# Kernel tuning notes

Measured on AMD Instinct MI355X. Metric: run time of the kernel, lower is better.

## Reference

```python
import jax, jax.numpy as jnp
import numpy as np

SEQ, B, OBS, H = 128, 256, 64, 1024

def setup_inputs() -> dict:
    key = jax.random.key(0)
    ks = jax.random.split(key, 16)
    s = 0.03  # keep weights small so tanh/sigmoid stay in a sane range
    n = lambda k, shape, sc=s: jax.random.normal(k, shape, jnp.float32) * sc
    return {
        "x": jax.random.normal(ks[0], (SEQ * B, OBS), jnp.float32),
        "done": jax.random.randint(ks[1], (SEQ * B,), 0, 2).astype(jnp.int32),
        "h0": n(ks[2], (2, B, H), 0.1),
        "c0": n(ks[3], (2, B, H), 0.1),
        "W_ih0": n(ks[4], (4 * H, OBS)),
        "W_hh0": n(ks[5], (4 * H, H)),
        "b_ih0": jnp.zeros((4 * H,), jnp.float32),
        "b_hh0": jnp.zeros((4 * H,), jnp.float32),
        "W_ih1": n(ks[6], (4 * H, H)),
        "W_hh1": n(ks[7], (4 * H, H)),
        "b_ih1": jnp.zeros((4 * H,), jnp.float32),
        "b_hh1": jnp.zeros((4 * H,), jnp.float32),
        "ln_g": jnp.ones((H,), jnp.float32),
        "ln_b": jnp.zeros((H,), jnp.float32),
        "W1": n(ks[8], (512, H)),
        "b1": jnp.zeros((512,), jnp.float32),
        "W2": n(ks[9], (128, 512)),
        "b2": jnp.zeros((128,), jnp.float32),
        "W3": n(ks[10], (64, 128)),
        "b3": jnp.zeros((64,), jnp.float32),
        "Wv": n(ks[11], (1, 64)),
        "bv": jnp.zeros((1,), jnp.float32),
    }

def _lstm_cell(xin, h, c, Wih, Whh, bih, bhh):
    # PyTorch gate order: input, forget, cell(g), output
    g = xin @ Wih.T + bih + h @ Whh.T + bhh
    i, f, gg, o = jnp.split(g, 4, axis=-1)
    c2 = jax.nn.sigmoid(f) * c + jax.nn.sigmoid(i) * jnp.tanh(gg)
    h2 = jax.nn.sigmoid(o) * jnp.tanh(c2)
    return h2, c2

def reference(x, done, h0, c0, W_ih0, W_hh0, b_ih0, b_hh0, W_ih1, W_hh1,
              b_ih1, b_hh1, ln_g, ln_b, W1, b1, W2, b2, W3, b3, Wv, bv):
    batch = h0.shape[1]
    obs = x.shape[-1]
    xs = x.reshape(-1, batch, obs)                      # (S, B, obs)
    ds = done.reshape(-1, batch).astype(x.dtype)        # (S, B)

    def step(carry, td):
        h, c = carry                                    # each (2, B, H)
        xt, dt = td
        m = (1.0 - dt)[:, None]                         # reset mask (B, 1)
        h0_, c0_ = _lstm_cell(xt, h[0] * m, c[0] * m, W_ih0, W_hh0, b_ih0, b_hh0)
        h1_, c1_ = _lstm_cell(h0_, h[1] * m, c[1] * m, W_ih1, W_hh1, b_ih1, b_hh1)
        return (jnp.stack([h0_, h1_]), jnp.stack([c0_, c1_])), h1_

    (hN, cN), hs = jax.lax.scan(step, (h0, c0), (xs, ds))
    hidden = hs.reshape(-1, hs.shape[-1])               # (S*B, H)

    # LayerNorm (eps = 1e-5, torch default)
    mu = hidden.mean(-1, keepdims=True)
    var = jnp.mean(jnp.square(hidden - mu), -1, keepdims=True)
    hn = (hidden - mu) * jax.lax.rsqrt(var + 1e-5) * ln_g + ln_b

    a = jax.nn.elu(hn @ W1.T + b1)
    a = jax.nn.elu(a @ W2.T + b2)
    a = jax.nn.elu(a @ W3.T + b3)
    value = a @ Wv.T + bv                               # (S*B, 1)
    return value, hN, cN
```

## Files before the change

kernel.cpp:

```cpp
#include <hip/hip_runtime.h>
#include <cstdint>
#include <cstddef>

typedef unsigned short u16;
typedef __attribute__((ext_vector_type(8))) short short8;
typedef __attribute__((ext_vector_type(4))) float f32x4;

#define SEQ 128
#define BATCH 256
#define HID 1024
#define LSZ 262144

#define MFMA(a,b,c) __builtin_amdgcn_mfma_f32_16x16x32_bf16((a),(b),(c),0,0,0)

#define GLDS_CG(g, l) __builtin_amdgcn_global_load_lds( \
  (__attribute__((address_space(1))) void*)(uintptr_t)(const void*)(g), \
  (__attribute__((address_space(3))) void*)(unsigned)(uintptr_t)(void*)(l), 16, 0, 17)
#define GLDS_NC(g, l) __builtin_amdgcn_global_load_lds( \
  (__attribute__((address_space(1))) void*)(uintptr_t)(const void*)(g), \
  (__attribute__((address_space(3))) void*)(unsigned)(uintptr_t)(void*)(l), 16, 0, 0)

__device__ __forceinline__ u16 f2b(float f) {
  union { float f; unsigned u; } v; v.f = f;
  unsigned r = (v.u + 0x7FFFu + ((v.u >> 16) & 1u)) >> 16;
  return (u16)r;
}
__device__ __forceinline__ float b2f(u16 h) {
  union { unsigned u; float f; } v; v.u = ((unsigned)h) << 16; return v.f;
}
__device__ __forceinline__ float sigm(float x){ return 1.f/(1.f + __expf(-x)); }
__device__ __forceinline__ float tanh_f(float x){
  x = fminf(15.f, fmaxf(-15.f, x));
  float e = __expf(2.f*x); return (e-1.f)/(e+1.f);
}
__device__ __forceinline__ float eluf(float x){ return x > 0.f ? x : expm1f(x); }

__device__ __forceinline__ void store_cg(u16* p, short8 v) {
  asm volatile("global_store_dwordx4 %0, %1, off sc0 sc1" :: "v"(p), "v"(v) : "memory");
}
__device__ __forceinline__ void wait_vm0() {
  asm volatile("s_waitcnt vmcnt(0)" ::: "memory");
}
__device__ __forceinline__ void waitgroup(int* f, int tgt) {
  if (threadIdx.x < 64) {
    int idx = threadIdx.x & 31;
    while (__hip_atomic_load(f + idx, __ATOMIC_RELAXED, __HIP_MEMORY_SCOPE_AGENT) < tgt)
      __builtin_amdgcn_s_sleep(1);
  }
  __syncthreads();
}

static const size_t OFF_W0F  = 0;
static const size_t OFF_W1F  = 8912896;
static const size_t OFF_XF   = 25690112;
static const size_t OFF_H0U  = 29884416;
static const size_t OFF_C0   = 30932992;
static const size_t OFF_C1   = 31981568;
static const size_t OFF_H1U  = 33030144;
static const size_t OFF_BS0  = 100663296;
static const size_t OFF_BS1  = 100679680;
static const size_t OFF_MU   = 100697088;
static const size_t OFF_RSTD = 100828160;
static const size_t OFF_W1LN = 100959232;
static const size_t OFF_S1   = 102007808;
static const size_t OFF_B1P  = 102009856;
static const size_t OFF_W2B  = 102011904;
static const size_t OFF_W3B  = 102142976;
static const size_t OFF_A1   = 102159360;
static const size_t OFF_A2   = 0;
static const size_t OFF_A3   = 8912896;
static const size_t OFF_H0M  = 102159360;
static const size_t OFF_H1M  = 102159360 + 1048576;

__global__ void prep_wf(const float* __restrict__ wih, const float* __restrict__ whh,
                        u16* __restrict__ out, int nkb, int kx) {
  int b = blockIdx.x; int cg = b >> 3, ct = b & 7;
  int g = ct >> 1;
  int n = nkb << 9;
  for (int e = threadIdx.x; e < n; e += 256) {
    int kb = e >> 9, r = e & 511;
    int q = r >> 7, col16 = (r >> 3) & 15, j = r & 7;
    int hl = (ct & 1) * 16 + col16;
    int gr = g * HID + cg * 32 + hl;
    int k = kb * 32 + q * 8 + j;
    float w = (k < kx) ? wih[(size_t)gr * kx + k] : whh[(size_t)gr * HID + (k - kx)];
    out[((size_t)(cg * nkb + kb) * 8 + ct) * 512 + r] = f2b(w);
  }
}

__global__ void prep_w1ln(const float* __restrict__ w1, const float* __restrict__ lng,
                          const float* __restrict__ lnb, const float* __restrict__ b1,
                          u16* __restrict__ w1ln, float* __restrict__ S1, float* __restrict__ b1p) {
  int j = blockIdx.x;
  float s = 0.f, bb = 0.f;
  for (int k = threadIdx.x; k < HID; k += 256) {
    float w = w1[(size_t)j * HID + k];
    u16 q = f2b(w * lng[k]);
    w1ln[(size_t)j * HID + k] = q;
    s += b2f(q);
    bb += w * lnb[k];
  }
  __shared__ float r1[256], r2[256];
  r1[threadIdx.x] = s; r2[threadIdx.x] = bb;
  __syncthreads();
  for (int o = 128; o > 0; o >>= 1) {
    if (threadIdx.x < (unsigned)o) { r1[threadIdx.x] += r1[threadIdx.x+o]; r2[threadIdx.x] += r2[threadIdx.x+o]; }
    __syncthreads();
  }
  if (threadIdx.x == 0) { S1[j] = r1[0]; b1p[j] = b1[j] + r2[0]; }
}

__global__ void prep_misc(const float* bih0, const float* bhh0, const float* bih1, const float* bhh1,
                          const float* x, const float* h0in, const float* c0in,
                          const float* w2, const float* w3, const int* done,
                          float* bs0, float* bs1, u16* xf, u16* h0m, u16* h1m,
                          float* c0buf, float* c1buf, u16* w2b, u16* w3b, int* flg) {
  size_t i = (size_t)blockIdx.x * blockDim.x + threadIdx.x;
  if (i < 4096) { bs0[i] = bih0[i] + bhh0[i]; return; }
  i -= 4096;
  if (i < 4096) { bs1[i] = bih1[i] + bhh1[i]; return; }
  i -= 4096;
  if (i < 2097152) {
    int o = (int)i;
    int r = o & 511, tile = o >> 9;
    int q = r >> 7, rl = (r >> 3) & 15, j = r & 7;
    int kb = tile & 1, v = tile >> 1;
    int grt = v & 15, t = v >> 4;
    int row = grt * 16 + rl, k = kb * 32 + q * 8 + j;
    xf[o] = f2b(x[((size_t)t * BATCH + row) * 64 + k]);
    return;
  }
  i -= 2097152;
  if (i < 262144) {
    int o = (int)i;
    int r = o & 511, tile = o >> 9;
    int q = r >> 7, rl = (r >> 3) & 15, j = r & 7;
    int grt = tile >> 5, kb = tile & 31;
    int row = grt * 16 + rl, h = kb * 32 + q * 8 + j;
    h0m[o] = done[row] ? (u16)0 : f2b(h0in[(size_t)row * HID + h]);
    return;
  }
  i -= 262144;
  if (i < 262144) {
    int o = (int)i;
    int r = o & 511, tile = o >> 9;
    int q = r >> 7, rl = (r >> 3) & 15, j = r & 7;
    int grt = tile >> 5, kb = tile & 31;
    int row = grt * 16 + rl, h = kb * 32 + q * 8 + j;
    h1m[o] = done[row] ? (u16)0 : f2b(h0in[LSZ + (size_t)row * HID + h]);
    return;
  }
  i -= 262144;
  if (i < LSZ) { c0buf[i] = c0in[i]; return; }
  i -= LSZ;
  if (i < LSZ) { c1buf[i] = c0in[LSZ + i]; return; }
  i -= LSZ;
  if (i < 65536) { w2b[i] = f2b(w2[i]); return; }
  i -= 65536;
  if (i < 8192) { w3b[i] = f2b(w3[i]); return; }
  i -= 8192;
  if (i < 512) { flg[i] = 0; return; }
}

__global__ __launch_bounds__(256, 2) void lstm_persist(
    const u16* __restrict__ w0f, const u16* __restrict__ w1f, const u16* __restrict__ xf,
    u16* __restrict__ h0u, u16* __restrict__ h1u,
    u16* __restrict__ h0m, u16* __restrict__ h1m,
    float* __restrict__ c0b, float* __restrict__ c1b,
    const float* __restrict__ bs0, const float* __restrict__ bs1,
    const int* __restrict__ done, int* __restrict__ flg,
    float* __restrict__ dout)
{
  const int bid = blockIdx.x;
  const int layer = bid >> 8;
  const int rg = (bid >> 5) & 7;
  const int cg = bid & 31;
  const int tid = threadIdx.x;
  const int lane = tid & 63, wv = tid >> 6;
  const int quad = lane >> 4, c16 = lane & 15;
  const int NKB = layer ? 64 : 34;
  const int NC  = layer ? 16 : 9;
  const u16* Wf = layer ? w1f : w0f;
  const float* bs = layer ? bs1 : bs0;
  float* cb = layer ? c1b : c0b;
  int* fl0 = flg;
  int* fl1 = flg + 256;
  int* myf = (layer ? fl1 : fl0) + rg * 32 + cg;
  int* g0 = fl0 + rg * 32;
  int* g1 = fl1 + rg * 32;

  __shared__ __align__(16) u16 smem[16384];
  float* gl = (float*)smem;

  const short8 z8 = {0,0,0,0,0,0,0,0};

  for (int t = 0; t < SEQ; ++t) {
    if (layer == 0) {
      if (t >= 1) waitgroup(g0, t);
    } else {
      if (t >= 1) waitgroup(g1, t);
    }

    auto ocmap = [&](int p) -> int {
      if (layer) return p >= 16 ? 7 : (p < 8 ? p + 8 : p - 8);
      return p > 8 ? 8 : p;
    };

    auto issueA = [&](int p) {
      int oc = ocmap(p);
      int kb = oc * 4 + wv; if (kb > NKB - 1) kb = NKB - 1;
      u16* lb = &smem[((unsigned)(p & 3)) * 4096 + (unsigned)wv * 1024];
      if (layer == 0) {
        if (kb < 2) {
          #pragma unroll
          for (int j = 0; j < 2; ++j) {
            const u16* g = xf + ((size_t)((t * 16 + rg * 2 + j) * 2 + kb)) * 512 + lane * 8;
            GLDS_NC(g, lb + j * 512);
          }
        } else {
          #pragma unroll
          for (int j = 0; j < 2; ++j) {
            const u16* g = h0m + (size_t)(t & 1) * 262144
                               + (size_t)((rg * 2 + j) * 32 + (kb - 2)) * 512 + lane * 8;
            GLDS_CG(g, lb + j * 512);
          }
        }
      } else {
        if (kb < 32) {
          #pragma unroll
          for (int j = 0; j < 2; ++j) {
            const u16* g = h0u + (size_t)((t + 1) & 1) * 262144
                               + (size_t)((rg * 2 + j) * 32 + kb) * 512 + lane * 8;
            GLDS_CG(g, lb + j * 512);
          }
        } else {
          #pragma unroll
          for (int j = 0; j < 2; ++j) {
            const u16* g = h1m + (size_t)(t & 1) * 262144
                               + (size_t)((rg * 2 + j) * 32 + (kb - 32)) * 512 + lane * 8;
            GLDS_CG(g, lb + j * 512);
          }
        }
      }
    };

    auto loadB = [&](int p, short8 (&vB)[4][2]) {
      int oc = ocmap(p);
      #pragma unroll
      for (int kbl = 0; kbl < 4; ++kbl) {
        int kb = oc * 4 + kbl; if (kb > NKB - 1) kb = NKB - 1;
        #pragma unroll
        for (int h = 0; h < 2; ++h)
          vB[kbl][h] = *(const short8*)(Wf + ((size_t)(cg * NKB + kb) * 8 + wv * 2 + h) * 512 + lane * 8);
      }
    };

    f32x4 acc[2][2];
    #pragma unroll
    for (int a = 0; a < 2; ++a) { acc[a][0] = (f32x4){0,0,0,0}; acc[a][1] = (f32x4){0,0,0,0}; }

    auto comp = [&](int p, short8 (&vB)[4][2]) {
      int oc = ocmap(p);
      int kbc = NKB - oc * 4; if (kbc > 4) kbc = 4;
      const u16* sb = &smem[((unsigned)(p & 3)) * 4096] + lane * 8;
      #pragma unroll
      for (int kbl = 0; kbl < 4; ++kbl) if (kbl < kbc) {
        #pragma unroll
        for (int a = 0; a < 2; ++a) {
          short8 af = *(const short8*)(sb + (kbl * 2 + a) * 512);
          acc[a][0] = MFMA(af, vB[kbl][0], acc[a][0]);
          acc[a][1] = MFMA(af, vB[kbl][1], acc[a][1]);
        }
      }
    };

    short8 vB0[4][2], vB1[4][2], vB2[4][2];

    loadB(0, vB0); issueA(0);
    asm volatile("" ::: "memory");
    loadB(1, vB1); issueA(1);

#define CHUNK(CC, VBL, VBU) \
    if (layer && (CC) == 6) waitgroup(g0, t + 1); \
    loadB((CC) + 2, VBL); issueA((CC) + 2); \
    asm volatile("s_waitcnt vmcnt(20)" ::: "memory"); \
    __builtin_amdgcn_s_barrier(); \
    __builtin_amdgcn_sched_barrier(0); \
    comp((CC), VBU);

    int c = 0;
    for (;;) {
      CHUNK(c, vB2, vB0) if (++c == NC) break;
      CHUNK(c, vB0, vB1) if (++c == NC) break;
      CHUNK(c, vB1, vB2) if (++c == NC) break;
    }
#undef CHUNK

    wait_vm0();
    __syncthreads();

    #pragma unroll
    for (int a = 0; a < 2; ++a)
      #pragma unroll
      for (int ct = 0; ct < 2; ++ct)
        #pragma unroll
        for (int rgi = 0; rgi < 4; ++rgi)
          gl[(a * 16 + quad * 4 + rgi) * 132 + wv * 32 + ct * 16 + c16] = acc[a][ct][rgi];
    __syncthreads();

    if (layer == 0 && t >= 2) waitgroup(g1, t - 1);

    if (tid < 128) {
      int row = tid >> 2;
      int q = tid & 3;
      int h8 = q * 8;
      int rowg = rg * 32 + row;
      int H0 = cg * 32 + h8;
      const float* glp = gl + row * 132;
      float m = done[t * BATCH + rowg] ? 0.f : 1.f;
      int nx = (t < SEQ - 1) ? done[(t + 1) * BATCH + rowg] : 0;
      float* cp = cb + (size_t)rowg * HID + H0;
      short8 hv;
      float h2a[8], c2a[8];
      #pragma unroll
      for (int j = 0; j < 8; ++j) {
        float ivv = glp[h8 + j]      + bs[H0 + j];
        float fvv = glp[32 + h8 + j] + bs[HID + H0 + j];
        float gvv = glp[64 + h8 + j] + bs[2*HID + H0 + j];
        float ovv = glp[96 + h8 + j] + bs[3*HID + H0 + j];
        float c2 = sigm(fvv) * (cp[j] * m) + sigm(ivv) * tanh_f(gvv);
        float h2 = sigm(ovv) * tanh_f(c2);
        cp[j] = c2;
        h2a[j] = h2; c2a[j] = c2;
        ((u16*)&hv)[j] = f2b(h2);
      }
      short8 hm = nx ? z8 : hv;
      size_t off = (size_t)((rg * 2 + (row >> 4)) * 32 + cg) * 512 + (size_t)(q * 16 + (row & 15)) * 8;
      if (layer == 0) {
        store_cg(h0u + (size_t)((t + 1) & 1) * 262144 + off, hv);
        if (t < SEQ - 1) store_cg(h0m + (size_t)((t + 1) & 1) * 262144 + off, hm);
      } else {
        store_cg(h1u + (size_t)(t + 1) * 262144 + off, hv);
        if (t < SEQ - 1) store_cg(h1m + (size_t)((t + 1) & 1) * 262144 + off, hm);
      }
      if (t == SEQ - 1) {
        float* dh = dout + 32768 + (size_t)layer * LSZ + (size_t)rowg * HID + H0;
        float* dc = dout + 32768 + 2 * LSZ + (size_t)layer * LSZ + (size_t)rowg * HID + H0;
        #pragma unroll
        for (int j = 0; j < 8; ++j) { dh[j] = h2a[j]; dc[j] = c2a[j]; }
      }
    }
    wait_vm0();
    __syncthreads();
    if (tid == 0) __hip_atomic_fetch_add(myf, 1, __ATOMIC_RELAXED, __HIP_MEMORY_SCOPE_AGENT);
  }
}

__global__ void ln_stats(const u16* __restrict__ h1u, float* __restrict__ mu, float* __restrict__ rstd) {
  int R = blockIdx.x * 4 + (threadIdx.x >> 6);
  int l = threadIdx.x & 63;
  int t = R >> 8, brow = R & 255, grt = brow >> 4, rl = brow & 15;
  const u16* base = h1u + (size_t)(t + 1) * 262144 + (size_t)(grt * 32 + (l >> 1)) * 512;
  int q2 = (l & 1) * 2;
  short8 v0 = *(const short8*)(base + (q2 * 16 + rl) * 8);
  short8 v1 = *(const short8*)(base + ((q2 + 1) * 16 + rl) * 8);
  float s = 0.f, q = 0.f;
  #pragma unroll
  for (int e = 0; e < 8; ++e) {
    float a = b2f((u16)v0[e]); s += a; q += a*a;
    float b = b2f((u16)v1[e]); s += b; q += b*b;
  }
  for (int o = 32; o > 0; o >>= 1) { s += __shfl_xor(s, o); q += __shfl_xor(q, o); }
  if (l == 0) {
    float mm = s * (1.f/1024.f);
    float var = q * (1.f/1024.f) - mm*mm;
    mu[R] = mm; rstd[R] = rsqrtf(var + 1e-5f);
  }
}

__global__ __launch_bounds__(512, 4) void mlp_gemm(
    const u16* __restrict__ A, int lda, int amode,
    const u16* __restrict__ B, int K, int N,
    u16* __restrict__ out, int ldo, int mode, int swiz,
    const float* __restrict__ mu, const float* __restrict__ rstd,
    const float* __restrict__ S1v, const float* __restrict__ bias)
{
  int nt, mtb;
  if (swiz) { int p = blockIdx.x * gridDim.y + blockIdx.y; nt = p & 3; mtb = p >> 2; }
  else { nt = blockIdx.x; mtb = blockIdx.y; }
  const int tid = threadIdx.x, lane = tid & 63, wv = tid >> 6;
  const int quad = lane >> 4, c16 = lane & 15;
  __shared__ __align__(16) u16 Am[16384], Bm[16384];
  f32x4 acc[8];
  #pragma unroll
  for (int i = 0; i < 8; ++i) acc[i] = (f32x4){0.f,0.f,0.f,0.f};

  int arow[4], akl[4], bcol[4];
  #pragma unroll
  for (int i = 0; i < 4; ++i) {
    int s = tid + i * 512, sub = s >> 6, lp = s & 63;
    int ks = sub >> 3, u = sub & 7;
    arow[i] = mtb * 128 + u * 16 + (lp & 15);
    akl[i]  = ks * 32 + (lp >> 4) * 8;
    bcol[i] = nt * 128 + u * 16 + (lp & 15);
  }
  short8 vA[4], vB[4];
  const short8 z8 = {0,0,0,0,0,0,0,0};
  const int NCH = K >> 7;
  auto load_stage = [&](int ci) {
    int kc = ci << 7;
    #pragma unroll
    for (int i = 0; i < 4; ++i) {
      if (amode) {
        int R = arow[i], k = kc + akl[i];
        const u16* p = A + (size_t)((R >> 8) + 1) * 262144
                         + (size_t)(((R >> 4) & 15) * 32 + (k >> 5)) * 512
                         + (size_t)((((k >> 3) & 3) * 16 + (R & 15)) * 8);
        vA[i] = *(const short8*)p;
      } else {
        vA[i] = *(const short8*)(A + (size_t)arow[i] * lda + kc + akl[i]);
      }
      vB[i] = (bcol[i] < N) ? *(const short8*)(B + (size_t)bcol[i] * K + kc + akl[i]) : z8;
    }
  };
  load_stage(0);
  for (int ci = 0; ci < NCH; ++ci) {
    #pragma unroll
    for (int i = 0; i < 4; ++i) {
      *(short8*)&Am[(size_t)(tid + i*512) * 8] = vA[i];
      *(short8*)&Bm[(size_t)(tid + i*512) * 8] = vB[i];
    }
    __syncthreads();
    if (ci + 1 < NCH) load_stage(ci + 1);
    #pragma unroll
    for (int ks = 0; ks < 4; ++ks) {
      short8 bf = *(const short8*)&Bm[((ks*8 + wv)*64 + lane) * 8];
      #pragma unroll
      for (int rt = 0; rt < 8; ++rt) {
        short8 af = *(const short8*)&Am[((ks*8 + rt)*64 + lane) * 8];
        acc[rt] = MFMA(af, bf, acc[rt]);
      }
    }
    __syncthreads();
  }
  int col = nt * 128 + wv * 16 + c16;
  if (col < N) {
    #pragma unroll
    for (int rt = 0; rt < 8; ++rt) {
      #pragma unroll
      for (int rgi = 0; rgi < 4; ++rgi) {
        int row = mtb * 128 + rt * 16 + quad * 4 + rgi;
        float v = acc[rt][rgi];
        if (mode == 0) v = v * rstd[row] - mu[row] * rstd[row] * S1v[col] + bias[col];
        else           v = v + bias[col];
        v = eluf(v);
        out[(size_t)row * ldo + col] = f2b(v);
      }
    }
  }
}

__global__ void value_head(const u16* __restrict__ a3, const float* __restrict__ wv,
                           const float* __restrict__ bv, float* __restrict__ dout) {
  int row = blockIdx.x * 256 + threadIdx.x;
  const short8* p = (const short8*)(a3 + (size_t)row * 64);
  float s = bv[0];
  #pragma unroll
  for (int j = 0; j < 8; ++j) {
    short8 v = p[j];
    #pragma unroll
    for (int e = 0; e < 8; ++e) s += b2f((u16)v[e]) * wv[j*8+e];
  }
  dout[row] = s;
}

extern "C" void kernel_launch(void* const* d_in, const int* in_sizes, int n_in,
                              void* d_out, int out_size, void* d_ws, size_t ws_size,
                              hipStream_t stream) {
  (void)in_sizes; (void)n_in; (void)out_size; (void)ws_size;
  const float* x    = (const float*)d_in[0];
  const int*   done = (const int*)d_in[1];
  const float* h0in = (const float*)d_in[2];
  const float* c0in = (const float*)d_in[3];
  const float* wih0 = (const float*)d_in[4];
  const float* whh0 = (const float*)d_in[5];
  const float* bih0 = (const float*)d_in[6];
  const float* bhh0 = (const float*)d_in[7];
  const float* wih1 = (const float*)d_in[8];
  const float* whh1 = (const float*)d_in[9];
  const float* bih1 = (const float*)d_in[10];
  const float* bhh1 = (const float*)d_in[11];
  const float* lng  = (const float*)d_in[12];
  const float* lnb  = (const float*)d_in[13];
  const float* w1   = (const float*)d_in[14];
  const float* b1   = (const float*)d_in[15];
  const float* w2   = (const float*)d_in[16];
  const float* b2   = (const float*)d_in[17];
  const float* w3   = (const float*)d_in[18];
  const float* b3   = (const float*)d_in[19];
  const float* wvp  = (const float*)d_in[20];
  const float* bvp  = (const float*)d_in[21];
  float* dout = (float*)d_out;
  char* ws = (char*)d_ws;

  u16*   w0f  = (u16*)(ws + OFF_W0F);
  u16*   w1f  = (u16*)(ws + OFF_W1F);
  u16*   xf   = (u16*)(ws + OFF_XF);
  u16*   h0u  = (u16*)(ws + OFF_H0U);
  u16*   h1u  = (u16*)(ws + OFF_H1U);
  u16*   h0m  = (u16*)(ws + OFF_H0M);
  u16*   h1m  = (u16*)(ws + OFF_H1M);
  float* c0b  = (float*)(ws + OFF_C0);
  float* c1b  = (float*)(ws + OFF_C1);
  float* bs0  = (float*)(ws + OFF_BS0);
  float* bs1  = (float*)(ws + OFF_BS1);
  int*   flg  = (int*)(ws + OFF_MU);
  float* mu   = (float*)(ws + OFF_MU);
  float* rstd = (float*)(ws + OFF_RSTD);
  u16*   w1ln = (u16*)(ws + OFF_W1LN);
  float* s1   = (float*)(ws + OFF_S1);
  float* b1p  = (float*)(ws + OFF_B1P);
  u16*   w2b  = (u16*)(ws + OFF_W2B);
  u16*   w3b  = (u16*)(ws + OFF_W3B);
  u16*   a1   = (u16*)(ws + OFF_A1);
  u16*   a2   = (u16*)(ws + OFF_A2);
  u16*   a3   = (u16*)(ws + OFF_A3);

  prep_wf<<<256, 256, 0, stream>>>(wih0, whh0, w0f, 34, 64);
  prep_wf<<<256, 256, 0, stream>>>(wih1, whh1, w1f, 64, 1024);
  prep_w1ln<<<512, 256, 0, stream>>>(w1, lng, lnb, b1, w1ln, s1, b1p);
  prep_misc<<<12610, 256, 0, stream>>>(bih0, bhh0, bih1, bhh1, x, h0in, c0in, w2, w3, done,
                                       bs0, bs1, xf, h0m, h1m, c0b, c1b, w2b, w3b, flg);

  lstm_persist<<<512, 256, 0, stream>>>(w0f, w1f, xf, h0u, h1u, h0m, h1m, c0b, c1b,
                                        bs0, bs1, done, flg, dout);

  ln_stats<<<8192, 256, 0, stream>>>(h1u, mu, rstd);
  mlp_gemm<<<dim3(8, 128), 512, 0, stream>>>(h1u, 0, 1, w1ln, 1024, 512, a1, 512, 0, 1, mu, rstd, s1, b1p);
  mlp_gemm<<<dim3(1, 256), 512, 0, stream>>>(a1, 512, 0, w2b, 512, 128, a2, 128, 1, 0, mu, rstd, s1, b2);
  mlp_gemm<<<dim3(1, 256), 512, 0, stream>>>(a2, 128, 0, w3b, 128, 64, a3, 64, 1, 0, mu, rstd, s1, b3);
  value_head<<<128, 256, 0, stream>>>(a3, wvp, bvp, dout);
}
```

Measured before the change: 2.742 ms.

## Double K-chunk size in persistent LSTM pipeline and restructure prefetch depth

Each pipeline chunk now covers 8 K-blocks instead of 4, halving the number of chunks per step. Weight fragments are double-buffered in registers with one-ahead prefetch, while activations stay two-ahead in a doubled LDS ring. Layer 1 now waits for layer 0's current step up front instead of mid-loop, and the group-wait barrier drops the full __syncthreads fence. This cuts per-chunk barrier and wait overhead, but raises register and LDS pressure and loses the reordered chunk mapping that let layer 1 overlap with layer 0.

New measurement: 2.730 ms (median of 2 runs). No clear change (-0.4%).

```diff
diff --git a/kernel.cpp b/kernel.cpp
--- a/kernel.cpp
+++ b/kernel.cpp
@@ -47,7 +47,9 @@
     while (__hip_atomic_load(f + idx, __ATOMIC_RELAXED, __HIP_MEMORY_SCOPE_AGENT) < tgt)
       __builtin_amdgcn_s_sleep(1);
   }
-  __syncthreads();
+  asm volatile("" ::: "memory");
+  __builtin_amdgcn_s_barrier();
+  __builtin_amdgcn_sched_barrier(0);
 }
 
 static const size_t OFF_W0F  = 0;
@@ -179,7 +181,7 @@
   const int lane = tid & 63, wv = tid >> 6;
   const int quad = lane >> 4, c16 = lane & 15;
   const int NKB = layer ? 64 : 34;
-  const int NC  = layer ? 16 : 9;
+  const int NC  = layer ? 8 : 5;
   const u16* Wf = layer ? w1f : w0f;
   const float* bs = layer ? bs1 : bs0;
   float* cb = layer ? c1b : c0b;
@@ -189,7 +191,7 @@
   int* g0 = fl0 + rg * 32;
   int* g1 = fl1 + rg * 32;
 
-  __shared__ __align__(16) u16 smem[16384];
+  __shared__ __align__(16) u16 smem[32768];
   float* gl = (float*)smem;
 
   const short8 z8 = {0,0,0,0,0,0,0,0};
@@ -198,57 +200,58 @@
     if (layer == 0) {
       if (t >= 1) waitgroup(g0, t);
     } else {
+      waitgroup(g0, t + 1);
       if (t >= 1) waitgroup(g1, t);
     }
 
-    auto ocmap = [&](int p) -> int {
-      if (layer) return p >= 16 ? 7 : (p < 8 ? p + 8 : p - 8);
-      return p > 8 ? 8 : p;
-    };
-
     auto issueA = [&](int p) {
-      int oc = ocmap(p);
-      int kb = oc * 4 + wv; if (kb > NKB - 1) kb = NKB - 1;
-      u16* lb = &smem[((unsigned)(p & 3)) * 4096 + (unsigned)wv * 1024];
-      if (layer == 0) {
-        if (kb < 2) {
-          #pragma unroll
-          for (int j = 0; j < 2; ++j) {
-            const u16* g = xf + ((size_t)((t * 16 + rg * 2 + j) * 2 + kb)) * 512 + lane * 8;
-            GLDS_NC(g, lb + j * 512);
+      int oc = p; if (oc > NC - 1) oc = NC - 1;
+      u16* lb = &smem[((unsigned)(p & 3)) * 8192];
+      #pragma unroll
+      for (int s = 0; s < 2; ++s) {
+        int kbl = wv + s * 4;
+        int kb = oc * 8 + kbl; if (kb > NKB - 1) kb = NKB - 1;
+        u16* lt = lb + (unsigned)(kbl * 2) * 512;
+        if (layer == 0) {
+          if (kb < 2) {
+            #pragma unroll
+            for (int j = 0; j < 2; ++j) {
+              const u16* g = xf + ((size_t)((t * 16 + rg * 2 + j) * 2 + kb)) * 512 + lane * 8;
+              GLDS_NC(g, lt + j * 512);
+            }
+          } else {
+            #pragma unroll
+            for (int j = 0; j < 2; ++j) {
+              const u16* g = h0m + (size_t)(t & 1) * 262144
+                                 + (size_t)((rg * 2 + j) * 32 + (kb - 2)) * 512 + lane * 8;
+              GLDS_CG(g, lt + j * 512);
+            }
           }
         } else {
-          #pragma unroll
-          for (int j = 0; j < 2; ++j) {
-            const u16* g = h0m + (size_t)(t & 1) * 262144
-                               + (size_t)((rg * 2 + j) * 32 + (kb - 2)) * 512 + lane * 8;
-            GLDS_CG(g, lb + j * 512);
+          if (kb < 32) {
+            #pragma unroll
+            for (int j = 0; j < 2; ++j) {
+              const u16* g = h0u + (size_t)((t + 1) & 1) * 262144
+                                 + (size_t)((rg * 2 + j) * 32 + kb) * 512 + lane * 8;
+              GLDS_CG(g, lt + j * 512);
+            }
+          } else {
+            #pragma unroll
+            for (int j = 0; j < 2; ++j) {
+              const u16* g = h1m + (size_t)(t & 1) * 262144
+                                 + (size_t)((rg * 2 + j) * 32 + (kb - 32)) * 512 + lane * 8;
+              GLDS_CG(g, lt + j * 512);
+            }
           }
         }
-      } else {
-        if (kb < 32) {
-          #pragma unroll
-          for (int j = 0; j < 2; ++j) {
-            const u16* g = h0u + (size_t)((t + 1) & 1) * 262144
-                               + (size_t)((rg * 2 + j) * 32 + kb) * 512 + lane * 8;
-            GLDS_CG(g, lb + j * 512);
-          }
-        } else {
-          #pragma unroll
-          for (int j = 0; j < 2; ++j) {
-            const u16* g = h1m + (size_t)(t & 1) * 262144
-                               + (size_t)((rg * 2 + j) * 32 + (kb - 32)) * 512 + lane * 8;
-            GLDS_CG(g, lb + j * 512);
-          }
-        }
       }
     };
 
-    auto loadB = [&](int p, short8 (&vB)[4][2]) {
-      int oc = ocmap(p);
-      #pragma unroll
-      for (int kbl = 0; kbl < 4; ++kbl) {
-        int kb = oc * 4 + kbl; if (kb > NKB - 1) kb = NKB - 1;
+    auto loadB = [&](int p, short8 (&vB)[8][2]) {
+      int oc = p; if (oc > NC - 1) oc = NC - 1;
+      #pragma unroll
+      for (int kbl = 0; kbl < 8; ++kbl) {
+        int kb = oc * 8 + kbl; if (kb > NKB - 1) kb = NKB - 1;
         #pragma unroll
         for (int h = 0; h < 2; ++h)
           vB[kbl][h] = *(const short8*)(Wf + ((size_t)(cg * NKB + kb) * 8 + wv * 2 + h) * 512 + lane * 8);
@@ -259,12 +262,11 @@
     #pragma unroll
     for (int a = 0; a < 2; ++a) { acc[a][0] = (f32x4){0,0,0,0}; acc[a][1] = (f32x4){0,0,0,0}; }
 
-    auto comp = [&](int p, short8 (&vB)[4][2]) {
-      int oc = ocmap(p);
-      int kbc = NKB - oc * 4; if (kbc > 4) kbc = 4;
-      const u16* sb = &smem[((unsigned)(p & 3)) * 4096] + lane * 8;
-      #pragma unroll
-      for (int kbl = 0; kbl < 4; ++kbl) if (kbl < kbc) {
+    auto comp = [&](int p, short8 (&vB)[8][2]) {
+      int kbc = NKB - p * 8; if (kbc > 8) kbc = 8;
+      const u16* sb = &smem[((unsigned)(p & 3)) * 8192] + lane * 8;
+      #pragma unroll
+      for (int kbl = 0; kbl < 8; ++kbl) if (kbl < kbc) {
         #pragma unroll
         for (int a = 0; a < 2; ++a) {
           short8 af = *(const short8*)(sb + (kbl * 2 + a) * 512);
@@ -274,25 +276,27 @@
       }
     };
 
-    short8 vB0[4][2], vB1[4][2], vB2[4][2];
-
-    loadB(0, vB0); issueA(0);
+    short8 vB0[8][2], vB1[8][2];
+
+    loadB(0, vB0);
     asm volatile("" ::: "memory");
-    loadB(1, vB1); issueA(1);
+    issueA(0);
+    asm volatile("" ::: "memory");
+    issueA(1);
 
 #define CHUNK(CC, VBL, VBU) \
-    if (layer && (CC) == 6) waitgroup(g0, t + 1); \
-    loadB((CC) + 2, VBL); issueA((CC) + 2); \
-    asm volatile("s_waitcnt vmcnt(20)" ::: "memory"); \
+    loadB((CC) + 1, VBL); \
+    asm volatile("" ::: "memory"); \
+    issueA((CC) + 2); \
+    asm volatile("s_waitcnt vmcnt(24)" ::: "memory"); \
     __builtin_amdgcn_s_barrier(); \
     __builtin_amdgcn_sched_barrier(0); \
     comp((CC), VBU);
 
     int c = 0;
     for (;;) {
-      CHUNK(c, vB2, vB0) if (++c == NC) break;
+      CHUNK(c, vB1, vB0) if (++c == NC) break;
       CHUNK(c, vB0, vB1) if (++c == NC) break;
-      CHUNK(c, vB1, vB2) if (++c == NC) break;
     }
 #undef CHUNK
 
```

## Deepen LSTM chunk pipeline and relax inter-layer synchronization with 4-slot h0 buffer

Applied to the files above, without the earlier changes.

Layer 1 now waits on both its own flags and layer 0's step t+1 flags together at the start of each step. This replaces the mid-loop wait and the reordered chunk map. The h0 buffer grows from two to four slots, so layer 0 only waits on layer 1 three steps back, which lets the two layers drift further apart. The K-chunk prefetch goes from two to three chunks ahead, with eight LDS slots and four B register sets, to hide more load latency. The cost is double the LDS use and more registers, which could reduce occupancy. Layer 1 also loses the chance to start on its own h1 chunks before layer 0 finishes.

Measured after the change: 2.778 ms. About the same (+1.3%).

```diff
diff --git a/kernel.cpp b/kernel.cpp
--- a/kernel.cpp
+++ b/kernel.cpp
@@ -47,13 +47,26 @@
     while (__hip_atomic_load(f + idx, __ATOMIC_RELAXED, __HIP_MEMORY_SCOPE_AGENT) < tgt)
       __builtin_amdgcn_s_sleep(1);
   }
-  __syncthreads();
+  asm volatile("" ::: "memory");
+  __builtin_amdgcn_s_barrier();
+  __builtin_amdgcn_sched_barrier(0);
+}
+__device__ __forceinline__ void waitgroup2(int* fa, int ta, int* fb, int tb) {
+  if (threadIdx.x < 64) {
+    int idx = threadIdx.x & 31;
+    int* p  = (threadIdx.x < 32) ? (fa + idx) : (fb + idx);
+    int tgt = (threadIdx.x < 32) ? ta : tb;
+    while (__hip_atomic_load(p, __ATOMIC_RELAXED, __HIP_MEMORY_SCOPE_AGENT) < tgt)
+      __builtin_amdgcn_s_sleep(1);
+  }
+  asm volatile("" ::: "memory");
+  __builtin_amdgcn_s_barrier();
+  __builtin_amdgcn_sched_barrier(0);
 }
 
 static const size_t OFF_W0F  = 0;
 static const size_t OFF_W1F  = 8912896;
 static const size_t OFF_XF   = 25690112;
-static const size_t OFF_H0U  = 29884416;
 static const size_t OFF_C0   = 30932992;
 static const size_t OFF_C1   = 31981568;
 static const size_t OFF_H1U  = 33030144;
@@ -71,6 +84,7 @@
 static const size_t OFF_A3   = 8912896;
 static const size_t OFF_H0M  = 102159360;
 static const size_t OFF_H1M  = 102159360 + 1048576;
+static const size_t OFF_H0U  = 102159360 + 2097152;
 
 __global__ void prep_wf(const float* __restrict__ wih, const float* __restrict__ whh,
                         u16* __restrict__ out, int nkb, int kx) {
@@ -189,7 +203,7 @@
   int* g0 = fl0 + rg * 32;
   int* g1 = fl1 + rg * 32;
 
-  __shared__ __align__(16) u16 smem[16384];
+  __shared__ __align__(16) u16 smem[32768];
   float* gl = (float*)smem;
 
   const short8 z8 = {0,0,0,0,0,0,0,0};
@@ -198,18 +212,14 @@
     if (layer == 0) {
       if (t >= 1) waitgroup(g0, t);
     } else {
-      if (t >= 1) waitgroup(g1, t);
-    }
-
-    auto ocmap = [&](int p) -> int {
-      if (layer) return p >= 16 ? 7 : (p < 8 ? p + 8 : p - 8);
-      return p > 8 ? 8 : p;
-    };
+      if (t >= 1) waitgroup2(g0, t + 1, g1, t);
+      else        waitgroup(g0, 1);
+    }
 
     auto issueA = [&](int p) {
-      int oc = ocmap(p);
+      int oc = p; if (oc > NC - 1) oc = NC - 1;
       int kb = oc * 4 + wv; if (kb > NKB - 1) kb = NKB - 1;
-      u16* lb = &smem[((unsigned)(p & 3)) * 4096 + (unsigned)wv * 1024];
+      u16* lb = &smem[((unsigned)(p & 7)) * 4096 + (unsigned)wv * 1024];
       if (layer == 0) {
         if (kb < 2) {
           #pragma unroll
@@ -229,7 +239,7 @@
         if (kb < 32) {
           #pragma unroll
           for (int j = 0; j < 2; ++j) {
-            const u16* g = h0u + (size_t)((t + 1) & 1) * 262144
+            const u16* g = h0u + (size_t)((t + 1) & 3) * 262144
                                + (size_t)((rg * 2 + j) * 32 + kb) * 512 + lane * 8;
             GLDS_CG(g, lb + j * 512);
           }
@@ -245,7 +255,7 @@
     };
 
     auto loadB = [&](int p, short8 (&vB)[4][2]) {
-      int oc = ocmap(p);
+      int oc = p; if (oc > NC - 1) oc = NC - 1;
       #pragma unroll
       for (int kbl = 0; kbl < 4; ++kbl) {
         int kb = oc * 4 + kbl; if (kb > NKB - 1) kb = NKB - 1;
@@ -260,9 +270,8 @@
     for (int a = 0; a < 2; ++a) { acc[a][0] = (f32x4){0,0,0,0}; acc[a][1] = (f32x4){0,0,0,0}; }
 
     auto comp = [&](int p, short8 (&vB)[4][2]) {
-      int oc = ocmap(p);
-      int kbc = NKB - oc * 4; if (kbc > 4) kbc = 4;
-      const u16* sb = &smem[((unsigned)(p & 3)) * 4096] + lane * 8;
+      int kbc = NKB - p * 4; if (kbc > 4) kbc = 4;
+      const u16* sb = &smem[((unsigned)(p & 7)) * 4096] + lane * 8;
       #pragma unroll
       for (int kbl = 0; kbl < 4; ++kbl) if (kbl < kbc) {
         #pragma unroll
@@ -274,25 +283,35 @@
       }
     };
 
-    short8 vB0[4][2], vB1[4][2], vB2[4][2];
-
-    loadB(0, vB0); issueA(0);
+    short8 vB0[4][2], vB1[4][2], vB2[4][2], vB3[4][2];
+
+    loadB(0, vB0);
     asm volatile("" ::: "memory");
-    loadB(1, vB1); issueA(1);
+    issueA(0);
+    asm volatile("" ::: "memory");
+    loadB(1, vB1);
+    asm volatile("" ::: "memory");
+    issueA(1);
+    asm volatile("" ::: "memory");
+    loadB(2, vB2);
+    asm volatile("" ::: "memory");
+    issueA(2);
 
 #define CHUNK(CC, VBL, VBU) \
-    if (layer && (CC) == 6) waitgroup(g0, t + 1); \
-    loadB((CC) + 2, VBL); issueA((CC) + 2); \
-    asm volatile("s_waitcnt vmcnt(20)" ::: "memory"); \
+    loadB((CC) + 3, VBL); \
+    asm volatile("" ::: "memory"); \
+    issueA((CC) + 3); \
+    asm volatile("s_waitcnt vmcnt(30)" ::: "memory"); \
     __builtin_amdgcn_s_barrier(); \
     __builtin_amdgcn_sched_barrier(0); \
     comp((CC), VBU);
 
     int c = 0;
     for (;;) {
-      CHUNK(c, vB2, vB0) if (++c == NC) break;
+      CHUNK(c, vB3, vB0) if (++c == NC) break;
       CHUNK(c, vB0, vB1) if (++c == NC) break;
       CHUNK(c, vB1, vB2) if (++c == NC) break;
+      CHUNK(c, vB2, vB3) if (++c == NC) break;
     }
 #undef CHUNK
 
@@ -308,7 +327,7 @@
           gl[(a * 16 + quad * 4 + rgi) * 132 + wv * 32 + ct * 16 + c16] = acc[a][ct][rgi];
     __syncthreads();
 
-    if (layer == 0 && t >= 2) waitgroup(g1, t - 1);
+    if (layer == 0 && t >= 4) waitgroup(g1, t - 3);
 
     if (tid < 128) {
       int row = tid >> 2;
@@ -337,7 +356,7 @@
       short8 hm = nx ? z8 : hv;
       size_t off = (size_t)((rg * 2 + (row >> 4)) * 32 + cg) * 512 + (size_t)(q * 16 + (row & 15)) * 8;
       if (layer == 0) {
-        store_cg(h0u + (size_t)((t + 1) & 1) * 262144 + off, hv);
+        store_cg(h0u + (size_t)((t + 1) & 3) * 262144 + off, hv);
         if (t < SEQ - 1) store_cg(h0m + (size_t)((t + 1) & 1) * 262144 + off, hm);
       } else {
         store_cg(h1u + (size_t)(t + 1) * 262144 + off, hv);
```
